# Optimization experiments

Hardware: AMD Instinct MI355X
Metric: run time of the kernel (lower is better)

## Reference

```python
import jax, jax.numpy as jnp
import numpy as np

N_NODES = 50000
N_EDGES = 800000
D = 128


def gcn_conv(x, src, dst, W, b, num_nodes):
    # PyG GCNConv: h = X W; add self-loops; symmetric deg^-1/2 normalization; scatter-add; + bias
    h = x @ W                                   # [N, F_out]
    ones = jnp.ones(src.shape[0], dtype=h.dtype)
    deg = jax.ops.segment_sum(ones, dst, num_segments=num_nodes)  # in-degree incl. self-loops
    dinv = jax.lax.rsqrt(jnp.maximum(deg, 1.0))  # deg >= 1 because of self-loops
    norm = dinv[src] * dinv[dst]                 # [E+N]
    msg = h[src] * norm[:, None]                 # gather + scale
    out = jax.ops.segment_sum(msg, dst, num_segments=num_nodes)
    return out + b


def setup_inputs() -> dict:
    key = jax.random.key(0)
    ks = jax.random.split(key, 6)
    x = jax.random.normal(ks[0], (N_NODES, D), dtype=jnp.float32)
    edge_index = jax.random.randint(ks[1], (2, N_EDGES), 0, N_NODES, dtype=jnp.int64)
    s = 1.0 / np.sqrt(D)
    W1 = jax.random.normal(ks[2], (D, D), dtype=jnp.float32) * s
    W2 = jax.random.normal(ks[3], (D, D), dtype=jnp.float32) * s
    Wg = jax.random.normal(ks[4], (2 * D, D), dtype=jnp.float32) * (1.0 / np.sqrt(2 * D))
    b1 = jnp.zeros((D,), jnp.float32)
    b2 = jnp.zeros((D,), jnp.float32)
    bg = jnp.zeros((D,), jnp.float32)
    return {"x": x, "edge_index": edge_index, "W1": W1, "b1": b1,
            "W2": W2, "b2": b2, "Wg": Wg, "bg": bg}


def reference(x, edge_index, W1, b1, W2, b2, Wg, bg):
    num_nodes = x.shape[0]
    x0 = jnp.clip(x, -100.0, 100.0)
    loop = jnp.arange(num_nodes, dtype=edge_index.dtype)
    src = jnp.concatenate([edge_index[0], loop])
    dst = jnp.concatenate([edge_index[1], loop])
    h = jax.nn.relu(gcn_conv(x0, src, dst, W1, b1, num_nodes))
    # F.dropout(p=0.3, training=False) -> identity at inference
    h = jax.nn.relu(gcn_conv(h, src, dst, W2, b2, num_nodes))
    h = h + x0  # residual (out_channels == in_channels)
    gate = jax.nn.sigmoid(jnp.concatenate([h, x0], axis=1) @ Wg + bg)
    return h * gate
```

## Files before the change

### kernel.cpp

```cpp
#include <hip/hip_runtime.h>
#include <hip/hip_bf16.h>

using short8 = __attribute__((ext_vector_type(8))) short;
using f32x4  = __attribute__((ext_vector_type(4))) float;

static constexpr int NN = 50000;
static constexpr int NE = 800000;
static constexpr int MPAD = 50048;
static constexpr int NB2 = 256;
static constexpr int BNODE = 196;
static constexpr int CAPB = 4096;
static constexpr int NCHB = 200;
static constexpr int CHB = NE / NCHB;

__device__ __forceinline__ float clip100(float v) { return fminf(fmaxf(v, -100.f), 100.f); }
__device__ __forceinline__ unsigned short f2b(float v) {
    __hip_bfloat16 h = __float2bfloat16(v);
    return *reinterpret_cast<unsigned short*>(&h);
}
__device__ __forceinline__ float blo(unsigned int u) { return __uint_as_float(u << 16); }
__device__ __forceinline__ float bhi(unsigned int u) { return __uint_as_float(u & 0xFFFF0000u); }
__device__ __forceinline__ float b2f(unsigned short u) {
    return __uint_as_float(((unsigned int)u) << 16);
}

__global__ __launch_bounds__(256) void k_front(const int* __restrict__ idx,
                                               int2* __restrict__ epair,
                                               int* __restrict__ gcur,
                                               const float* __restrict__ W1,
                                               const float* __restrict__ W2,
                                               const float* __restrict__ Wg,
                                               unsigned short* __restrict__ Wt1,
                                               unsigned short* __restrict__ Wt2,
                                               unsigned short* __restrict__ Wgt) {
    __shared__ int ls[CHB], ld[CHB];
    __shared__ int bcnt[NB2], bb[NB2], bofs[NB2];
    const int tid = threadIdx.x;
    if (blockIdx.x < NCHB) {
        const int beg = blockIdx.x * CHB;
        for (int i = tid; i < CHB; i += 256) {
            ls[i] = idx[beg + i];
            ld[i] = idx[NE + beg + i];
        }
        bcnt[tid] = 0;
        __syncthreads();
        for (int i = tid; i < CHB; i += 256) atomicAdd(&bcnt[ld[i] / BNODE], 1);
        __syncthreads();
        bb[tid] = atomicAdd(&gcur[tid], bcnt[tid]);
        bofs[tid] = 0;
        __syncthreads();
        for (int i = tid; i < CHB; i += 256) {
            const int d = ld[i];
            const int p = d / BNODE;
            const int pos = atomicAdd(&bofs[p], 1);
            epair[p * CAPB + bb[p] + pos] = make_int2(ls[i], d);
        }
    } else {
        const int i = (blockIdx.x - NCHB) * 256 + tid;
        if (i < 16384) {
            const int n = i >> 7, k = i & 127;
            Wt1[i] = f2b(W1[k * 128 + n]);
        } else if (i < 32768) {
            const int j = i - 16384;
            const int n = j >> 7, k = j & 127;
            Wt2[j] = f2b(W2[k * 128 + n]);
        } else {
            const int j = i - 32768;
            const int n = j >> 8, k = j & 255;
            Wgt[j] = f2b(Wg[k * 128 + n]);
        }
    }
}

__global__ __launch_bounds__(256) void k_mid(const int2* __restrict__ epair,
                                             const int* __restrict__ gcur,
                                             int* __restrict__ rowptr,
                                             float* __restrict__ dinv,
                                             int* __restrict__ esrc,
                                             const float* __restrict__ x,
                                             const unsigned short* __restrict__ Wt,
                                             unsigned short* __restrict__ Cb) {
    __shared__ alignas(16) char smem[CAPB * 3 * 4 + 3 * 256 * 4];
    const int tid = threadIdx.x;
    if (blockIdx.x < NB2) {
        int* ls   = (int*)smem;
        int* ld   = ls + CAPB;
        int* srt  = ld + CAPB;
        int* cntL = srt + CAPB;
        int* sc   = cntL + 256;
        int* cur  = sc + 256;
        const int t = tid;
        const int b = blockIdx.x;
        sc[t] = gcur[t];
        __syncthreads();
        for (int off = 1; off < 256; off <<= 1) {
            const int add = (t >= off) ? sc[t - off] : 0;
            __syncthreads();
            sc[t] += add;
            __syncthreads();
        }
        const int ne = gcur[b];
        const int base = sc[b] - ne;
        const int nb0 = b * BNODE;
        const int nn = min(NN - nb0, BNODE);
        if (b == 0 && t == 0) rowptr[NN] = NE;

        for (int i = t; i < ne; i += 256) {
            const int2 p = epair[b * CAPB + i];
            ls[i] = p.x;
            ld[i] = p.y - nb0;
        }
        cntL[t] = 0;
        __syncthreads();
        for (int i = t; i < ne; i += 256) atomicAdd(&cntL[ld[i]], 1);
        __syncthreads();
        sc[t] = cntL[t];
        __syncthreads();
        for (int off = 1; off < 256; off <<= 1) {
            const int add = (t >= off) ? sc[t - off] : 0;
            __syncthreads();
            sc[t] += add;
            __syncthreads();
        }
        const int excl = sc[t] - cntL[t];
        cur[t] = excl;
        if (t < nn) {
            rowptr[nb0 + t] = base + excl;
            dinv[nb0 + t] = rsqrtf(1.f + (float)cntL[t]);
        }
        __syncthreads();
        for (int i = t; i < ne; i += 256) {
            const int pos = atomicAdd(&cur[ld[i]], 1);
            srt[pos] = ls[i];
        }
        __syncthreads();
        for (int i = t; i < ne; i += 256) esrc[base + i] = srt[i];
    } else {
        unsigned short* wl = (unsigned short*)smem;
#pragma unroll
        for (int j = tid; j < 2048; j += 256) {
            const int row = j >> 4, c8 = j & 15;
            *(short8*)(wl + row * 136 + c8 * 8) = *(const short8*)(Wt + row * 128 + c8 * 8);
        }
        __syncthreads();

        const int wv = tid >> 6;
        const int ln = tid & 63;
        const int l16 = ln & 15;
        const int qd = ln >> 4;
        const int rowb = (blockIdx.x - NB2) * 64 + wv * 16;
        const long arow = rowb + l16;
        const int kq = qd * 8;

        f32x4 acc[8];
#pragma unroll
        for (int i = 0; i < 8; ++i) acc[i] = (f32x4){0.f, 0.f, 0.f, 0.f};

#pragma unroll
        for (int kc = 0; kc < 4; ++kc) {
            short8 a = (short8){0, 0, 0, 0, 0, 0, 0, 0};
            if (arow < NN) {
                const float* fp = x + arow * 128 + kc * 32 + kq;
                const float4 f0 = *(const float4*)fp;
                const float4 f1 = *(const float4*)(fp + 4);
                a[0] = (short)f2b(clip100(f0.x));
                a[1] = (short)f2b(clip100(f0.y));
                a[2] = (short)f2b(clip100(f0.z));
                a[3] = (short)f2b(clip100(f0.w));
                a[4] = (short)f2b(clip100(f1.x));
                a[5] = (short)f2b(clip100(f1.y));
                a[6] = (short)f2b(clip100(f1.z));
                a[7] = (short)f2b(clip100(f1.w));
            }
#pragma unroll
            for (int nt = 0; nt < 8; ++nt) {
                const short8 b = *(const short8*)(wl + (nt * 16 + l16) * 136 + kc * 32 + kq);
                acc[nt] = __builtin_amdgcn_mfma_f32_16x16x32_bf16(a, b, acc[nt], 0, 0, 0);
            }
        }

        const int r0 = rowb + qd * 4;
#pragma unroll
        for (int r = 0; r < 4; ++r) {
            const int row = r0 + r;
            if (row < NN) {
#pragma unroll
                for (int nt = 0; nt < 8; ++nt) {
                    Cb[(long)row * 128 + nt * 16 + l16] = f2b(acc[nt][r]);
                }
            }
        }
    }
}

__global__ __launch_bounds__(256) void k_mfma2(const unsigned short* __restrict__ Ab,
                                               const unsigned short* __restrict__ Wt,
                                               unsigned short* __restrict__ Cb,
                                               const float* __restrict__ dinv) {
    __shared__ unsigned short wl[128 * 136];
    const int tid = threadIdx.x;
#pragma unroll
    for (int j = tid; j < 2048; j += 256) {
        const int row = j >> 4, c8 = j & 15;
        *(short8*)(wl + row * 136 + c8 * 8) = *(const short8*)(Wt + row * 128 + c8 * 8);
    }
    __syncthreads();

    const int wv = tid >> 6;
    const int ln = tid & 63;
    const int l16 = ln & 15;
    const int qd = ln >> 4;
    const int rowb = blockIdx.x * 64 + wv * 16;
    const long arow = rowb + l16;
    const int kq = qd * 8;

    f32x4 acc[8];
#pragma unroll
    for (int i = 0; i < 8; ++i) acc[i] = (f32x4){0.f, 0.f, 0.f, 0.f};

#pragma unroll
    for (int kc = 0; kc < 4; ++kc) {
        const short8 a = *(const short8*)(Ab + arow * 128 + kc * 32 + kq);
#pragma unroll
        for (int nt = 0; nt < 8; ++nt) {
            const short8 b = *(const short8*)(wl + (nt * 16 + l16) * 136 + kc * 32 + kq);
            acc[nt] = __builtin_amdgcn_mfma_f32_16x16x32_bf16(a, b, acc[nt], 0, 0, 0);
        }
    }

    const int r0 = rowb + qd * 4;
#pragma unroll
    for (int r = 0; r < 4; ++r) {
        const int row = r0 + r;
        if (row < NN) {
            const float dv = dinv[row];
#pragma unroll
            for (int nt = 0; nt < 8; ++nt) {
                Cb[(long)row * 128 + nt * 16 + l16] = f2b(acc[nt][r] * dv);
            }
        }
    }
}

__global__ __launch_bounds__(256) void k_mfma_gate(const unsigned short* __restrict__ Ab,
                                                   const float* __restrict__ Af,
                                                   const unsigned short* __restrict__ Wt,
                                                   const float* __restrict__ bg,
                                                   float* __restrict__ out) {
    __shared__ unsigned short wl[128 * 136];
    const int tid = threadIdx.x;
    const int wv = tid >> 6;
    const int ln = tid & 63;
    const int l16 = ln & 15;
    const int qd = ln >> 4;
    const int rowb = blockIdx.x * 64 + wv * 16;
    const long arow = rowb + l16;
    const int kq = qd * 8;

    f32x4 acc[8];
#pragma unroll
    for (int i = 0; i < 8; ++i) acc[i] = (f32x4){0.f, 0.f, 0.f, 0.f};

#pragma unroll
    for (int j = tid; j < 2048; j += 256) {
        const int row = j >> 4, c8 = j & 15;
        *(short8*)(wl + row * 136 + c8 * 8) = *(const short8*)(Wt + row * 256 + c8 * 8);
    }
    __syncthreads();
    {
        const unsigned short* ap = Ab + arow * 128 + kq;
#pragma unroll
        for (int kc = 0; kc < 4; ++kc) {
            const short8 a = *(const short8*)(ap + kc * 32);
#pragma unroll
            for (int nt = 0; nt < 8; ++nt) {
                const short8 b = *(const short8*)(wl + (nt * 16 + l16) * 136 + kc * 32 + kq);
                acc[nt] = __builtin_amdgcn_mfma_f32_16x16x32_bf16(a, b, acc[nt], 0, 0, 0);
            }
        }
    }
    __syncthreads();

#pragma unroll
    for (int j = tid; j < 2048; j += 256) {
        const int row = j >> 4, c8 = j & 15;
        *(short8*)(wl + row * 136 + c8 * 8) = *(const short8*)(Wt + row * 256 + 128 + c8 * 8);
    }
    __syncthreads();
    {
        const bool valid = arow < NN;
        const float* fp = Af + arow * 128 + kq;
#pragma unroll
        for (int kc = 0; kc < 4; ++kc) {
            short8 a = (short8){0, 0, 0, 0, 0, 0, 0, 0};
            if (valid) {
                const float4 f0 = *(const float4*)(fp + kc * 32);
                const float4 f1 = *(const float4*)(fp + kc * 32 + 4);
                a[0] = (short)f2b(clip100(f0.x));
                a[1] = (short)f2b(clip100(f0.y));
                a[2] = (short)f2b(clip100(f0.z));
                a[3] = (short)f2b(clip100(f0.w));
                a[4] = (short)f2b(clip100(f1.x));
                a[5] = (short)f2b(clip100(f1.y));
                a[6] = (short)f2b(clip100(f1.z));
                a[7] = (short)f2b(clip100(f1.w));
            }
#pragma unroll
            for (int nt = 0; nt < 8; ++nt) {
                const short8 b = *(const short8*)(wl + (nt * 16 + l16) * 136 + kc * 32 + kq);
                acc[nt] = __builtin_amdgcn_mfma_f32_16x16x32_bf16(a, b, acc[nt], 0, 0, 0);
            }
        }
    }

    const int r0 = rowb + qd * 4;
#pragma unroll
    for (int nt = 0; nt < 8; ++nt) {
        const int col = nt * 16 + l16;
        const float bgv = bg[col];
#pragma unroll
        for (int r = 0; r < 4; ++r) {
            const int row = r0 + r;
            if (row < NN) {
                const float g = 1.f / (1.f + __expf(-(acc[nt][r] + bgv)));
                out[(long)row * 128 + col] = b2f(Ab[(long)row * 128 + col]) * g;
            }
        }
    }
}

template <bool RES, bool ESCALE>
__global__ __launch_bounds__(256) void k_aggr(const unsigned int* __restrict__ As2,
                                              unsigned short* __restrict__ Bb,
                                              const int* __restrict__ rowptr,
                                              const int* __restrict__ esrc,
                                              const float* __restrict__ dinv,
                                              const float* __restrict__ bias,
                                              const float* __restrict__ x) {
    const int d = __builtin_amdgcn_readfirstlane((blockIdx.x * 256 + threadIdx.x) >> 6);
    if (d >= NN) return;
    const int lane = threadIdx.x & 63;
    const float dd = dinv[d];

    const unsigned int u = As2[(long)d * 64 + lane];
    float2 acc;
    if (ESCALE) {
        acc.x = blo(u) * dd;
        acc.y = bhi(u) * dd;
    } else {
        acc.x = blo(u);
        acc.y = bhi(u);
    }

    const int beg = rowptr[d];
    const int end = rowptr[d + 1];
    int i = beg;
    for (; i + 8 <= end; i += 8) {
        const int s0 = esrc[i + 0], s1 = esrc[i + 1], s2 = esrc[i + 2], s3 = esrc[i + 3];
        const int s4 = esrc[i + 4], s5 = esrc[i + 5], s6 = esrc[i + 6], s7 = esrc[i + 7];
        const unsigned int v0 = As2[(long)s0 * 64 + lane];
        const unsigned int v1 = As2[(long)s1 * 64 + lane];
        const unsigned int v2 = As2[(long)s2 * 64 + lane];
        const unsigned int v3 = As2[(long)s3 * 64 + lane];
        const unsigned int v4 = As2[(long)s4 * 64 + lane];
        const unsigned int v5 = As2[(long)s5 * 64 + lane];
        const unsigned int v6 = As2[(long)s6 * 64 + lane];
        const unsigned int v7 = As2[(long)s7 * 64 + lane];
        if (ESCALE) {
            const float w0 = dinv[s0], w1 = dinv[s1], w2 = dinv[s2], w3 = dinv[s3];
            const float w4 = dinv[s4], w5 = dinv[s5], w6 = dinv[s6], w7 = dinv[s7];
            acc.x += ((blo(v0) * w0 + blo(v1) * w1) + (blo(v2) * w2 + blo(v3) * w3)) +
                     ((blo(v4) * w4 + blo(v5) * w5) + (blo(v6) * w6 + blo(v7) * w7));
            acc.y += ((bhi(v0) * w0 + bhi(v1) * w1) + (bhi(v2) * w2 + bhi(v3) * w3)) +
                     ((bhi(v4) * w4 + bhi(v5) * w5) + (bhi(v6) * w6 + bhi(v7) * w7));
        } else {
            acc.x += ((blo(v0) + blo(v1)) + (blo(v2) + blo(v3))) +
                     ((blo(v4) + blo(v5)) + (blo(v6) + blo(v7)));
            acc.y += ((bhi(v0) + bhi(v1)) + (bhi(v2) + bhi(v3))) +
                     ((bhi(v4) + bhi(v5)) + (bhi(v6) + bhi(v7)));
        }
    }
    if (i + 4 <= end) {
        const int s0 = esrc[i + 0], s1 = esrc[i + 1], s2 = esrc[i + 2], s3 = esrc[i + 3];
        const unsigned int v0 = As2[(long)s0 * 64 + lane];
        const unsigned int v1 = As2[(long)s1 * 64 + lane];
        const unsigned int v2 = As2[(long)s2 * 64 + lane];
        const unsigned int v3 = As2[(long)s3 * 64 + lane];
        if (ESCALE) {
            const float w0 = dinv[s0], w1 = dinv[s1], w2 = dinv[s2], w3 = dinv[s3];
            acc.x += (blo(v0) * w0 + blo(v1) * w1) + (blo(v2) * w2 + blo(v3) * w3);
            acc.y += (bhi(v0) * w0 + bhi(v1) * w1) + (bhi(v2) * w2 + bhi(v3) * w3);
        } else {
            acc.x += (blo(v0) + blo(v1)) + (blo(v2) + blo(v3));
            acc.y += (bhi(v0) + bhi(v1)) + (bhi(v2) + bhi(v3));
        }
        i += 4;
    }
    for (; i < end; ++i) {
        const int s = esrc[i];
        const unsigned int v = As2[(long)s * 64 + lane];
        if (ESCALE) {
            const float w = dinv[s];
            acc.x = fmaf(blo(v), w, acc.x);
            acc.y = fmaf(bhi(v), w, acc.y);
        } else {
            acc.x += blo(v);
            acc.y += bhi(v);
        }
    }

    const float2 bv = ((const float2*)bias)[lane];
    acc.x = fmaxf(fmaf(acc.x, dd, bv.x), 0.f);
    acc.y = fmaxf(fmaf(acc.y, dd, bv.y), 0.f);
    if (RES) {
        const float2 xv = ((const float2*)x)[(long)d * 64 + lane];
        acc.x += clip100(xv.x);
        acc.y += clip100(xv.y);
    }
    const unsigned int pack = (unsigned int)f2b(acc.x) | ((unsigned int)f2b(acc.y) << 16);
    ((unsigned int*)Bb)[(long)d * 64 + lane] = pack;
}

extern "C" void kernel_launch(void* const* d_in, const int* in_sizes, int n_in,
                              void* d_out, int out_size, void* d_ws, size_t ws_size,
                              hipStream_t stream) {
    const float* x  = (const float*)d_in[0];
    const int*  eix = (const int*)d_in[1];
    const float* W1 = (const float*)d_in[2];
    const float* b1 = (const float*)d_in[3];
    const float* W2 = (const float*)d_in[4];
    const float* b2 = (const float*)d_in[5];
    const float* Wg = (const float*)d_in[6];
    const float* bg = (const float*)d_in[7];
    float* out = (float*)d_out;

    char* ws = (char*)d_ws;
    unsigned short* As   = (unsigned short*)ws;
    unsigned short* hb   = (unsigned short*)(ws + 12812288);
    unsigned short* Wt1  = (unsigned short*)(ws + 25624576);
    unsigned short* Wt2  = (unsigned short*)(ws + 25657344);
    unsigned short* Wgt  = (unsigned short*)(ws + 25690112);
    int*   rowptr = (int*)(ws + 25755648);
    float* dinv   = (float*)(ws + 25956352);
    int*   gcur   = (int*)(ws + 26157056);
    int*   esrc   = (int*)(ws + 26159104);
    int2*  epair  = (int2*)(ws + 29359104);

    const int ggrid = MPAD / 64;
    dim3 blk(256);

    hipMemsetAsync(gcur, 0, NB2 * sizeof(int), stream);

    k_front<<<NCHB + 256, blk, 0, stream>>>(eix, epair, gcur, W1, W2, Wg, Wt1, Wt2, Wgt);

    k_mid<<<NB2 + ggrid, blk, 0, stream>>>(epair, gcur, rowptr, dinv, esrc, x, Wt1, As);

    k_aggr<false, true><<<(NN * 64 + 255) / 256, blk, 0, stream>>>(
        (const unsigned int*)As, hb, rowptr, esrc, dinv, b1, nullptr);

    k_mfma2<<<ggrid, blk, 0, stream>>>(hb, Wt2, As, dinv);

    k_aggr<true, false><<<(NN * 64 + 255) / 256, blk, 0, stream>>>(
        (const unsigned int*)As, hb, rowptr, esrc, dinv, b2, x);

    k_mfma_gate<<<ggrid, blk, 0, stream>>>(hb, x, Wgt, bg, out);
}
```

Before: 213.5 us.

## Store node features in 32-column slabs and aggregate four edges per wave

Intermediate bf16 feature matrices are stored as four column slabs of 32 features each, so one node's slab row is 64 bytes. The MFMA kernels write and read this layout. The aggregation kernel is restructured so each block handles one slab for a group of nodes, with each wave's four 16-lane quarters gathering different edges and combining results via cross-lane shuffles. The aim is a smaller per-feature gather working set that fits better in cache, at the cost of more index and dinv loads, select logic and shuffles per edge.

```diff
diff --git a/kernel.cpp b/kernel.cpp
--- a/kernel.cpp
+++ b/kernel.cpp
@@ -12,6 +12,9 @@
 static constexpr int CAPB = 4096;
 static constexpr int NCHB = 200;
 static constexpr int CHB = NE / NCHB;
+static constexpr int SLABN = MPAD * 32;
+static constexpr int SLABW = SLABN / 2;
+static constexpr int AGGRID = 12512;
 
 __device__ __forceinline__ float clip100(float v) { return fminf(fmaxf(v, -100.f), 100.f); }
 __device__ __forceinline__ unsigned short f2b(float v) {
@@ -186,7 +189,8 @@
             if (row < NN) {
 #pragma unroll
                 for (int nt = 0; nt < 8; ++nt) {
-                    Cb[(long)row * 128 + nt * 16 + l16] = f2b(acc[nt][r]);
+                    Cb[(long)(nt >> 1) * SLABN + (long)row * 32 + (nt & 1) * 16 + l16] =
+                        f2b(acc[nt][r]);
                 }
             }
         }
@@ -220,7 +224,7 @@
 
 #pragma unroll
     for (int kc = 0; kc < 4; ++kc) {
-        const short8 a = *(const short8*)(Ab + arow * 128 + kc * 32 + kq);
+        const short8 a = *(const short8*)(Ab + (long)kc * SLABN + arow * 32 + kq);
 #pragma unroll
         for (int nt = 0; nt < 8; ++nt) {
             const short8 b = *(const short8*)(wl + (nt * 16 + l16) * 136 + kc * 32 + kq);
@@ -236,7 +240,8 @@
             const float dv = dinv[row];
 #pragma unroll
             for (int nt = 0; nt < 8; ++nt) {
-                Cb[(long)row * 128 + nt * 16 + l16] = f2b(acc[nt][r] * dv);
+                Cb[(long)(nt >> 1) * SLABN + (long)row * 32 + (nt & 1) * 16 + l16] =
+                    f2b(acc[nt][r] * dv);
             }
         }
     }
@@ -268,10 +273,9 @@
     }
     __syncthreads();
     {
-        const unsigned short* ap = Ab + arow * 128 + kq;
 #pragma unroll
         for (int kc = 0; kc < 4; ++kc) {
-            const short8 a = *(const short8*)(ap + kc * 32);
+            const short8 a = *(const short8*)(Ab + (long)kc * SLABN + arow * 32 + kq);
 #pragma unroll
             for (int nt = 0; nt < 8; ++nt) {
                 const short8 b = *(const short8*)(wl + (nt * 16 + l16) * 136 + kc * 32 + kq);
@@ -323,102 +327,135 @@
             const int row = r0 + r;
             if (row < NN) {
                 const float g = 1.f / (1.f + __expf(-(acc[nt][r] + bgv)));
-                out[(long)row * 128 + col] = b2f(Ab[(long)row * 128 + col]) * g;
+                const unsigned short hu =
+                    Ab[(long)(nt >> 1) * SLABN + (long)row * 32 + (nt & 1) * 16 + l16];
+                out[(long)row * 128 + col] = b2f(hu) * g;
             }
         }
     }
 }
 
 template <bool RES, bool ESCALE>
-__global__ __launch_bounds__(256) void k_aggr(const unsigned int* __restrict__ As2,
-                                              unsigned short* __restrict__ Bb,
+__global__ __launch_bounds__(256) void k_aggr(const unsigned short* __restrict__ As,
+                                              unsigned short* __restrict__ Hb,
                                               const int* __restrict__ rowptr,
                                               const int* __restrict__ esrc,
                                               const float* __restrict__ dinv,
                                               const float* __restrict__ bias,
                                               const float* __restrict__ x) {
-    const int d = __builtin_amdgcn_readfirstlane((blockIdx.x * 256 + threadIdx.x) >> 6);
-    if (d >= NN) return;
+    const int k   = (blockIdx.x & 7) >> 1;
+    const int ngp = ((blockIdx.x >> 3) << 1) | (blockIdx.x & 1);
     const int lane = threadIdx.x & 63;
-    const float dd = dinv[d];
-
-    const unsigned int u = As2[(long)d * 64 + lane];
-    float2 acc;
-    if (ESCALE) {
-        acc.x = blo(u) * dd;
-        acc.y = bhi(u) * dd;
-    } else {
-        acc.x = blo(u);
-        acc.y = bhi(u);
-    }
-
-    const int beg = rowptr[d];
-    const int end = rowptr[d + 1];
-    int i = beg;
-    for (; i + 8 <= end; i += 8) {
-        const int s0 = esrc[i + 0], s1 = esrc[i + 1], s2 = esrc[i + 2], s3 = esrc[i + 3];
-        const int s4 = esrc[i + 4], s5 = esrc[i + 5], s6 = esrc[i + 6], s7 = esrc[i + 7];
-        const unsigned int v0 = As2[(long)s0 * 64 + lane];
-        const unsigned int v1 = As2[(long)s1 * 64 + lane];
-        const unsigned int v2 = As2[(long)s2 * 64 + lane];
-        const unsigned int v3 = As2[(long)s3 * 64 + lane];
-        const unsigned int v4 = As2[(long)s4 * 64 + lane];
-        const unsigned int v5 = As2[(long)s5 * 64 + lane];
-        const unsigned int v6 = As2[(long)s6 * 64 + lane];
-        const unsigned int v7 = As2[(long)s7 * 64 + lane];
+    const int q  = lane >> 4;
+    const int fp = lane & 15;
+    const unsigned int* Ak = (const unsigned int*)As + (long)k * SLABW;
+    unsigned int* Hk = (unsigned int*)Hb + (long)k * SLABW;
+    const float2 bv = ((const float2*)(bias + k * 32))[fp];
+
+    const int d0 = ngp * 16 + (threadIdx.x >> 6) * 4;
+#pragma unroll 1
+    for (int j = 0; j < 4; ++j) {
+        const int d = __builtin_amdgcn_readfirstlane(d0 + j);
+        if (d >= NN) continue;
+        const float dd = dinv[d];
+        const int beg = rowptr[d];
+        const int end = rowptr[d + 1];
+        float ax = 0.f, ay = 0.f;
+        int i = beg;
+        for (; i + 8 <= end; i += 8) {
+            const int s0 = esrc[i + 0], s1 = esrc[i + 1], s2 = esrc[i + 2], s3 = esrc[i + 3];
+            const int s4 = esrc[i + 4], s5 = esrc[i + 5], s6 = esrc[i + 6], s7 = esrc[i + 7];
+            {
+                const int sa = (q & 1) ? s1 : s0;
+                const int sb = (q & 1) ? s3 : s2;
+                const int sv = (q & 2) ? sb : sa;
+                const unsigned int u = Ak[(long)sv * 16 + fp];
+                if (ESCALE) {
+                    const float wa = (q & 1) ? dinv[s1] : dinv[s0];
+                    const float wb = (q & 1) ? dinv[s3] : dinv[s2];
+                    const float w = (q & 2) ? wb : wa;
+                    ax = fmaf(blo(u), w, ax);
+                    ay = fmaf(bhi(u), w, ay);
+                } else {
+                    ax += blo(u);
+                    ay += bhi(u);
+                }
+            }
+            {
+                const int sa = (q & 1) ? s5 : s4;
+                const int sb = (q & 1) ? s7 : s6;
+                const int sv = (q & 2) ? sb : sa;
+                const unsigned int u = Ak[(long)sv * 16 + fp];
+                if (ESCALE) {
+                    const float wa = (q & 1) ? dinv[s5] : dinv[s4];
+                    const float wb = (q & 1) ? dinv[s7] : dinv[s6];
+                    const float w = (q & 2) ? wb : wa;
+                    ax = fmaf(blo(u), w, ax);
+                    ay = fmaf(bhi(u), w, ay);
+                } else {
+                    ax += blo(u);
+                    ay += bhi(u);
+                }
+            }
+        }
+        if (i + 4 <= end) {
+            const int s0 = esrc[i + 0], s1 = esrc[i + 1], s2 = esrc[i + 2], s3 = esrc[i + 3];
+            const int sa = (q & 1) ? s1 : s0;
+            const int sb = (q & 1) ? s3 : s2;
+            const int sv = (q & 2) ? sb : sa;
+            const unsigned int u = Ak[(long)sv * 16 + fp];
+            if (ESCALE) {
+                const float wa = (q & 1) ? dinv[s1] : dinv[s0];
+                const float wb = (q & 1) ? dinv[s3] : dinv[s2];
+                const float w = (q & 2) ? wb : wa;
+                ax = fmaf(blo(u), w, ax);
+                ay = fmaf(bhi(u), w, ay);
+            } else {
+                ax += blo(u);
+                ay += bhi(u);
+            }
+            i += 4;
+        }
+        const int r = end - i;
+        if (r > 0) {
+            const int s0 = esrc[i];
+            const int s1 = esrc[i + ((r > 1) ? 1 : 0)];
+            const int s2 = esrc[i + ((r > 2) ? 2 : 0)];
+            const int sa = (q & 1) ? s1 : s0;
+            const int sv = (q & 2) ? s2 : sa;
+            const unsigned int u = Ak[(long)sv * 16 + fp];
+            float w = (q < r) ? 1.f : 0.f;
+            if (ESCALE) {
+                const float wa = (q & 1) ? dinv[s1] : dinv[s0];
+                const float wsv = (q & 2) ? dinv[s2] : wa;
+                w *= wsv;
+            }
+            ax = fmaf(blo(u), w, ax);
+            ay = fmaf(bhi(u), w, ay);
+        }
+        ax += __shfl_xor(ax, 16);
+        ax += __shfl_xor(ax, 32);
+        ay += __shfl_xor(ay, 16);
+        ay += __shfl_xor(ay, 32);
+        const unsigned int us = Ak[(long)d * 16 + fp];
         if (ESCALE) {
-            const float w0 = dinv[s0], w1 = dinv[s1], w2 = dinv[s2], w3 = dinv[s3];
-            const float w4 = dinv[s4], w5 = dinv[s5], w6 = dinv[s6], w7 = dinv[s7];
-            acc.x += ((blo(v0) * w0 + blo(v1) * w1) + (blo(v2) * w2 + blo(v3) * w3)) +
-                     ((blo(v4) * w4 + blo(v5) * w5) + (blo(v6) * w6 + blo(v7) * w7));
-            acc.y += ((bhi(v0) * w0 + bhi(v1) * w1) + (bhi(v2) * w2 + bhi(v3) * w3)) +
-                     ((bhi(v4) * w4 + bhi(v5) * w5) + (bhi(v6) * w6 + bhi(v7) * w7));
+            ax = fmaf(blo(us), dd, ax);
+            ay = fmaf(bhi(us), dd, ay);
         } else {
-            acc.x += ((blo(v0) + blo(v1)) + (blo(v2) + blo(v3))) +
-                     ((blo(v4) + blo(v5)) + (blo(v6) + blo(v7)));
-            acc.y += ((bhi(v0) + bhi(v1)) + (bhi(v2) + bhi(v3))) +
-                     ((bhi(v4) + bhi(v5)) + (bhi(v6) + bhi(v7)));
-        }
-    }
-    if (i + 4 <= end) {
-        const int s0 = esrc[i + 0], s1 = esrc[i + 1], s2 = esrc[i + 2], s3 = esrc[i + 3];
-        const unsigned int v0 = As2[(long)s0 * 64 + lane];
-        const unsigned int v1 = As2[(long)s1 * 64 + lane];
-        const unsigned int v2 = As2[(long)s2 * 64 + lane];
-        const unsigned int v3 = As2[(long)s3 * 64 + lane];
-        if (ESCALE) {
-            const float w0 = dinv[s0], w1 = dinv[s1], w2 = dinv[s2], w3 = dinv[s3];
-            acc.x += (blo(v0) * w0 + blo(v1) * w1) + (blo(v2) * w2 + blo(v3) * w3);
-            acc.y += (bhi(v0) * w0 + bhi(v1) * w1) + (bhi(v2) * w2 + bhi(v3) * w3);
-        } else {
-            acc.x += (blo(v0) + blo(v1)) + (blo(v2) + blo(v3));
-            acc.y += (bhi(v0) + bhi(v1)) + (bhi(v2) + bhi(v3));
-        }
-        i += 4;
-    }
-    for (; i < end; ++i) {
-        const int s = esrc[i];
-        const unsigned int v = As2[(long)s * 64 + lane];
-        if (ESCALE) {
-            const float w = dinv[s];
-            acc.x = fmaf(blo(v), w, acc.x);
-            acc.y = fmaf(bhi(v), w, acc.y);
-        } else {
-            acc.x += blo(v);
-            acc.y += bhi(v);
-        }
-    }
-
-    const float2 bv = ((const float2*)bias)[lane];
-    acc.x = fmaxf(fmaf(acc.x, dd, bv.x), 0.f);
-    acc.y = fmaxf(fmaf(acc.y, dd, bv.y), 0.f);
-    if (RES) {
-        const float2 xv = ((const float2*)x)[(long)d * 64 + lane];
-        acc.x += clip100(xv.x);
-        acc.y += clip100(xv.y);
-    }
-    const unsigned int pack = (unsigned int)f2b(acc.x) | ((unsigned int)f2b(acc.y) << 16);
-    ((unsigned int*)Bb)[(long)d * 64 + lane] = pack;
+            ax += blo(us);
+            ay += bhi(us);
+        }
+        float fx = fmaxf(fmaf(ax, dd, bv.x), 0.f);
+        float fy = fmaxf(fmaf(ay, dd, bv.y), 0.f);
+        if (RES) {
+            const float2 xv = ((const float2*)(x + (long)d * 128 + k * 32))[fp];
+            fx += clip100(xv.x);
+            fy += clip100(xv.y);
+        }
+        if (lane < 16) {
+            Hk[(long)d * 16 + fp] = (unsigned int)f2b(fx) | ((unsigned int)f2b(fy) << 16);
+        }
+    }
 }
 
 extern "C" void kernel_launch(void* const* d_in, const int* in_sizes, int n_in,
@@ -455,13 +492,13 @@
 
     k_mid<<<NB2 + ggrid, blk, 0, stream>>>(epair, gcur, rowptr, dinv, esrc, x, Wt1, As);
 
-    k_aggr<false, true><<<(NN * 64 + 255) / 256, blk, 0, stream>>>(
-        (const unsigned int*)As, hb, rowptr, esrc, dinv, b1, nullptr);
+    k_aggr<false, true><<<AGGRID, blk, 0, stream>>>(
+        As, hb, rowptr, esrc, dinv, b1, nullptr);
 
     k_mfma2<<<ggrid, blk, 0, stream>>>(hb, Wt2, As, dinv);
 
-    k_aggr<true, false><<<(NN * 64 + 255) / 256, blk, 0, stream>>>(
-        (const unsigned int*)As, hb, rowptr, esrc, dinv, b2, x);
+    k_aggr<true, false><<<AGGRID, blk, 0, stream>>>(
+        As, hb, rowptr, esrc, dinv, b2, x);
 
     k_mfma_gate<<<ggrid, blk, 0, stream>>>(hb, x, Wgt, bg, out);
 }
```

New measurement: 267.1 us. 1.25x slower.
